# Optimization experiments

Measured on AMD Instinct MI355X. Metric: run time of the kernel, lower is better.

Reference implementation:

```python
import jax, jax.numpy as jnp
import numpy as np

N_JOINTS = 50
N_BONES = 50
# getSkeletalModelStructure() stand-in: 50 bones over 50 joints (i -> (i+1) % 50)
SRC = jnp.arange(N_BONES)
DST = (jnp.arange(N_BONES) + 1) % N_JOINTS
EPS = 1e-8


def _length_direct(x):
    # x: [B, T, 150] -> lengths [B, T, 50], directions [B, T, 150]
    B, T, _ = x.shape
    joints = x.reshape(B, T, N_JOINTS, 3)
    diff = joints[:, :, SRC, :] - joints[:, :, DST, :]      # [B, T, 50, 3]
    length = jnp.sqrt(jnp.sum(diff * diff, axis=-1))        # [B, T, 50]
    direct = diff / (length[..., None] + EPS)               # [B, T, 50, 3]
    return length, direct.reshape(B, T, N_BONES * 3)


def setup_inputs() -> dict:
    key = jax.random.key(0)
    k1, k2 = jax.random.split(key)
    preds = jax.random.normal(k1, (128, 1024, 150), dtype=jnp.float32)
    targets = jax.random.normal(k2, (128, 1024, 150), dtype=jnp.float32)
    return {"preds": preds, "targets": targets}


def reference(preds, targets):
    target_pad = 0.0
    loss_mask = (targets != target_pad).astype(jnp.float32)
    preds_masked = preds * loss_mask
    targets_masked = targets * loss_mask
    _, pd = _length_direct(preds_masked)
    _, td = _length_direct(targets_masked)
    pd = pd * loss_mask[:, :, :150]
    td = td * loss_mask[:, :, :150]
    # criterion = L1 (mean), criterion_bone = MSE (mean); loss_scale = 1.0
    loss = jnp.mean(jnp.abs(preds_masked - targets_masked)) + 0.1 * jnp.mean((pd - td) ** 2)
    return loss
```

## Files before the change

kernel.cpp:

```cpp
#include <hip/hip_runtime.h>


#define ROW_F   150
#define ROWS_PB 32
#define SPAN_F  (ROWS_PB * ROW_F)
#define SPAN_F4 (SPAN_F / 4)
#define N_CHUNK 19

typedef const __attribute__((address_space(1))) float  gfloat;
typedef __attribute__((address_space(3))) float        lfloat;

__global__ __launch_bounds__(256, 4) void loss_kernel(
    const float* __restrict__ preds,
    const float* __restrict__ targets,
    float* __restrict__ out,
    float inv_count)
{
    const float EPS = 1e-8f;
    __shared__ float sp[SPAN_F];
    __shared__ float st[SPAN_F];

    const int tid  = threadIdx.x;
    const int lane = tid & 63;
    const int wid  = tid >> 6;
    const size_t base = (size_t)blockIdx.x * SPAN_F;

    const float* gp = preds + base;
    const float* gt = targets + base;

    for (int c = wid; c < N_CHUNK; c += 4) {
        const int f4 = c * 64;
        if (f4 + lane < SPAN_F4) {
            __builtin_amdgcn_global_load_lds(
                (gfloat*)(gp + 4 * (f4 + lane)), (lfloat*)(sp + 4 * f4), 16, 0, 0);
            __builtin_amdgcn_global_load_lds(
                (gfloat*)(gt + 4 * (f4 + lane)), (lfloat*)(st + 4 * f4), 16, 0, 0);
        }
    }
    __syncthreads();

    const int seg = tid >> 5;
    const int row = tid & 31;
    const int j0 = (seg < 2) ? seg * 7 : 14 + (seg - 2) * 6;
    const int j1 = (seg < 2) ? j0 + 7  : j0 + 6;

    const float* rpb = sp + row * ROW_F;
    const float* rtb = st + row * ROW_F;

    float l1 = 0.0f, mse = 0.0f;

    auto load_joint = [&](int j, float* pm, float* tm, float* m) {
#pragma unroll
        for (int c = 0; c < 3; ++c) {
            float t = rtb[3 * j + c];
            float p = rpb[3 * j + c];
            float mk = (t != 0.0f) ? 1.0f : 0.0f;
            m[c] = mk;
            pm[c] = p * mk;
            tm[c] = t;
        }
    };

    auto do_bone = [&](const float* pmS, const float* tmS, const float* mS,
                       const float* pmD, const float* tmD) {
        float dp[3], dt[3];
        float lp = 0.0f, lt = 0.0f;
#pragma unroll
        for (int c = 0; c < 3; ++c) {
            dp[c] = pmS[c] - pmD[c];
            dt[c] = tmS[c] - tmD[c];
            lp += dp[c] * dp[c];
            lt += dt[c] * dt[c];
        }
        float ip = 1.0f / (sqrtf(lp) + EPS);
        float it = 1.0f / (sqrtf(lt) + EPS);
#pragma unroll
        for (int c = 0; c < 3; ++c) {
            float d = (dp[c] * ip - dt[c] * it) * mS[c];
            mse += d * d;
        }
    };

    float pmP[3], tmP[3], mP[3];
    load_joint(j0, pmP, tmP, mP);
#pragma unroll
    for (int c = 0; c < 3; ++c) l1 += fabsf(pmP[c] - tmP[c]);

    for (int b = j0; b < j1; ++b) {
        int jn = b + 1;
        if (jn == 50) jn = 0;
        float pmN[3], tmN[3], mN[3];
        load_joint(jn, pmN, tmN, mN);
        if (jn < j1 && jn != 0) {
#pragma unroll
            for (int c = 0; c < 3; ++c) l1 += fabsf(pmN[c] - tmN[c]);
        }
        do_bone(pmP, tmP, mP, pmN, tmN);
#pragma unroll
        for (int c = 0; c < 3; ++c) { pmP[c] = pmN[c]; tmP[c] = tmN[c]; mP[c] = mN[c]; }
    }

    float part = (l1 + 0.1f * mse) * inv_count;
#pragma unroll
    for (int off = 32; off > 0; off >>= 1)
        part += __shfl_down(part, off, 64);

    __shared__ float wsum[4];
    if (lane == 0) wsum[wid] = part;
    __syncthreads();
    if (tid == 0) {
        float s = wsum[0] + wsum[1] + wsum[2] + wsum[3];
        atomicAdd(out, s);
    }
}

extern "C" void kernel_launch(void* const* d_in, const int* in_sizes, int n_in,
                              void* d_out, int out_size, void* d_ws, size_t ws_size,
                              hipStream_t stream)
{
    const float* preds   = (const float*)d_in[0];
    const float* targets = (const float*)d_in[1];
    float* out = (float*)d_out;

    hipMemsetAsync(out, 0, sizeof(float) * out_size, stream);

    int n_elems = in_sizes[0];
    int n_rows  = n_elems / ROW_F;
    float inv_count = 1.0f / (float)n_elems;

    int grid = n_rows / ROWS_PB;
    loss_kernel<<<grid, 256, 0, stream>>>(preds, targets, out, inv_count);
}
```

Measured before the change: 184.3 us.

## Make loss kernel persistent with double-buffered LDS prefetch of spans

```diff
diff --git a/kernel.cpp b/kernel.cpp
--- a/kernel.cpp
+++ b/kernel.cpp
@@ -10,94 +10,107 @@
 typedef const __attribute__((address_space(1))) float  gfloat;
 typedef __attribute__((address_space(3))) float        lfloat;
 
-__global__ __launch_bounds__(256, 4) void loss_kernel(
+__device__ __forceinline__ void load_joint(const float* __restrict__ rpb,
+                                           const float* __restrict__ rtb,
+                                           int j, float* pm, float* tm, float* m)
+{
+#pragma unroll
+    for (int c = 0; c < 3; ++c) {
+        float t = rtb[3 * j + c];
+        float p = rpb[3 * j + c];
+        float mk = (t != 0.0f) ? 1.0f : 0.0f;
+        m[c] = mk;
+        pm[c] = p * mk;
+        tm[c] = t;
+    }
+}
+
+__device__ __forceinline__ void do_bone(const float* pmS, const float* tmS, const float* mS,
+                                        const float* pmD, const float* tmD, float& mse)
+{
+    const float EPS = 1e-8f;
+    float dp[3], dt[3];
+    float lp = 0.0f, lt = 0.0f;
+#pragma unroll
+    for (int c = 0; c < 3; ++c) {
+        dp[c] = pmS[c] - pmD[c];
+        dt[c] = tmS[c] - tmD[c];
+        lp += dp[c] * dp[c];
+        lt += dt[c] * dt[c];
+    }
+    float ip = 1.0f / (sqrtf(lp) + EPS);
+    float it = 1.0f / (sqrtf(lt) + EPS);
+#pragma unroll
+    for (int c = 0; c < 3; ++c) {
+        float d = (dp[c] * ip - dt[c] * it) * mS[c];
+        mse += d * d;
+    }
+}
+
+__global__ __launch_bounds__(256, 2) void loss_kernel(
     const float* __restrict__ preds,
     const float* __restrict__ targets,
     float* __restrict__ out,
-    float inv_count)
+    int iters, float inv_count)
 {
-    const float EPS = 1e-8f;
-    __shared__ float sp[SPAN_F];
-    __shared__ float st[SPAN_F];
+    __shared__ float smem[2][2][SPAN_F];
+    __shared__ float wsum[4];
 
     const int tid  = threadIdx.x;
     const int lane = tid & 63;
     const int wid  = tid >> 6;
-    const size_t base = (size_t)blockIdx.x * SPAN_F;
 
-    const float* gp = preds + base;
-    const float* gt = targets + base;
-
-    for (int c = wid; c < N_CHUNK; c += 4) {
-        const int f4 = c * 64;
-        if (f4 + lane < SPAN_F4) {
-            __builtin_amdgcn_global_load_lds(
-                (gfloat*)(gp + 4 * (f4 + lane)), (lfloat*)(sp + 4 * f4), 16, 0, 0);
-            __builtin_amdgcn_global_load_lds(
-                (gfloat*)(gt + 4 * (f4 + lane)), (lfloat*)(st + 4 * f4), 16, 0, 0);
+    auto stage = [&](int span, int buf) {
+        const float* gp = preds   + (size_t)span * SPAN_F;
+        const float* gt = targets + (size_t)span * SPAN_F;
+        float* bsp = smem[buf][0];
+        float* bst = smem[buf][1];
+        for (int c = wid; c < N_CHUNK; c += 4) {
+            const int f4 = c * 64;
+            if (f4 + lane < SPAN_F4) {
+                __builtin_amdgcn_global_load_lds(
+                    (gfloat*)(gp + 4 * (f4 + lane)), (lfloat*)(bsp + 4 * f4), 16, 0, 0);
+                __builtin_amdgcn_global_load_lds(
+                    (gfloat*)(gt + 4 * (f4 + lane)), (lfloat*)(bst + 4 * f4), 16, 0, 0);
+            }
         }
-    }
-    __syncthreads();
+    };
 
     const int seg = tid >> 5;
     const int row = tid & 31;
     const int j0 = (seg < 2) ? seg * 7 : 14 + (seg - 2) * 6;
     const int j1 = (seg < 2) ? j0 + 7  : j0 + 6;
 
-    const float* rpb = sp + row * ROW_F;
-    const float* rtb = st + row * ROW_F;
-
     float l1 = 0.0f, mse = 0.0f;
 
-    auto load_joint = [&](int j, float* pm, float* tm, float* m) {
+    stage(blockIdx.x, 0);
+
+    for (int it = 0; it < iters; ++it) {
+        __syncthreads();
+        if (it + 1 < iters)
+            stage(blockIdx.x + (it + 1) * gridDim.x, (it + 1) & 1);
+
+        const float* rpb = smem[it & 1][0] + row * ROW_F;
+        const float* rtb = smem[it & 1][1] + row * ROW_F;
+
+        float pmP[3], tmP[3], mP[3];
+        load_joint(rpb, rtb, j0, pmP, tmP, mP);
 #pragma unroll
-        for (int c = 0; c < 3; ++c) {
-            float t = rtb[3 * j + c];
-            float p = rpb[3 * j + c];
-            float mk = (t != 0.0f) ? 1.0f : 0.0f;
-            m[c] = mk;
-            pm[c] = p * mk;
-            tm[c] = t;
+        for (int c = 0; c < 3; ++c) l1 += fabsf(pmP[c] - tmP[c]);
+
+        for (int b = j0; b < j1; ++b) {
+            int jn = b + 1;
+            if (jn == 50) jn = 0;
+            float pmN[3], tmN[3], mN[3];
+            load_joint(rpb, rtb, jn, pmN, tmN, mN);
+            if (jn < j1 && jn != 0) {
+#pragma unroll
+                for (int c = 0; c < 3; ++c) l1 += fabsf(pmN[c] - tmN[c]);
+            }
+            do_bone(pmP, tmP, mP, pmN, tmN, mse);
+#pragma unroll
+            for (int c = 0; c < 3; ++c) { pmP[c] = pmN[c]; tmP[c] = tmN[c]; mP[c] = mN[c]; }
         }
-    };
-
-    auto do_bone = [&](const float* pmS, const float* tmS, const float* mS,
-                       const float* pmD, const float* tmD) {
-        float dp[3], dt[3];
-        float lp = 0.0f, lt = 0.0f;
-#pragma unroll
-        for (int c = 0; c < 3; ++c) {
-            dp[c] = pmS[c] - pmD[c];
-            dt[c] = tmS[c] - tmD[c];
-            lp += dp[c] * dp[c];
-            lt += dt[c] * dt[c];
-        }
-        float ip = 1.0f / (sqrtf(lp) + EPS);
-        float it = 1.0f / (sqrtf(lt) + EPS);
-#pragma unroll
-        for (int c = 0; c < 3; ++c) {
-            float d = (dp[c] * ip - dt[c] * it) * mS[c];
-            mse += d * d;
-        }
-    };
-
-    float pmP[3], tmP[3], mP[3];
-    load_joint(j0, pmP, tmP, mP);
-#pragma unroll
-    for (int c = 0; c < 3; ++c) l1 += fabsf(pmP[c] - tmP[c]);
-
-    for (int b = j0; b < j1; ++b) {
-        int jn = b + 1;
-        if (jn == 50) jn = 0;
-        float pmN[3], tmN[3], mN[3];
-        load_joint(jn, pmN, tmN, mN);
-        if (jn < j1 && jn != 0) {
-#pragma unroll
-            for (int c = 0; c < 3; ++c) l1 += fabsf(pmN[c] - tmN[c]);
-        }
-        do_bone(pmP, tmP, mP, pmN, tmN);
-#pragma unroll
-        for (int c = 0; c < 3; ++c) { pmP[c] = pmN[c]; tmP[c] = tmN[c]; mP[c] = mN[c]; }
     }
 
     float part = (l1 + 0.1f * mse) * inv_count;
@@ -105,7 +118,6 @@
     for (int off = 32; off > 0; off >>= 1)
         part += __shfl_down(part, off, 64);
 
-    __shared__ float wsum[4];
     if (lane == 0) wsum[wid] = part;
     __syncthreads();
     if (tid == 0) {
@@ -126,8 +138,10 @@
 
     int n_elems = in_sizes[0];
     int n_rows  = n_elems / ROW_F;
+    int spans   = n_rows / ROWS_PB;
     float inv_count = 1.0f / (float)n_elems;
 
-    int grid = n_rows / ROWS_PB;
-    loss_kernel<<<grid, 256, 0, stream>>>(preds, targets, out, inv_count);
+    int grid  = 512;
+    int iters = spans / grid;
+    loss_kernel<<<grid, 256, 0, stream>>>(preds, targets, out, iters, inv_count);
 }
```

Result: faster. 176.3 us (-4.3%).

## Make kernel persistent with register-prefetched spans and fast rcp/sqrt

Applied to the files above, without the earlier changes.

```diff
diff --git a/kernel.cpp b/kernel.cpp
--- a/kernel.cpp
+++ b/kernel.cpp
@@ -1,103 +1,114 @@
 #include <hip/hip_runtime.h>
 
 
-#define ROW_F   150
-#define ROWS_PB 32
-#define SPAN_F  (ROWS_PB * ROW_F)
-#define SPAN_F4 (SPAN_F / 4)
-#define N_CHUNK 19
-
-typedef const __attribute__((address_space(1))) float  gfloat;
-typedef __attribute__((address_space(3))) float        lfloat;
+#define ROW_F    150
+#define ROWS_PB  32
+#define SPAN_F   (ROWS_PB * ROW_F)
+#define SPAN_F4  (SPAN_F / 4)
+#define GRID     1024
 
 __global__ __launch_bounds__(256, 4) void loss_kernel(
     const float* __restrict__ preds,
     const float* __restrict__ targets,
     float* __restrict__ out,
-    float inv_count)
+    int iters, float inv_count)
 {
     const float EPS = 1e-8f;
     __shared__ float sp[SPAN_F];
     __shared__ float st[SPAN_F];
+    __shared__ float wsum[4];
 
     const int tid  = threadIdx.x;
     const int lane = tid & 63;
     const int wid  = tid >> 6;
-    const size_t base = (size_t)blockIdx.x * SPAN_F;
 
-    const float* gp = preds + base;
-    const float* gt = targets + base;
+    const float4* gp4 = reinterpret_cast<const float4*>(preds);
+    const float4* gt4 = reinterpret_cast<const float4*>(targets);
+    float4* sp4 = reinterpret_cast<float4*>(sp);
+    float4* st4 = reinterpret_cast<float4*>(st);
 
-    for (int c = wid; c < N_CHUNK; c += 4) {
-        const int f4 = c * 64;
-        if (f4 + lane < SPAN_F4) {
-            __builtin_amdgcn_global_load_lds(
-                (gfloat*)(gp + 4 * (f4 + lane)), (lfloat*)(sp + 4 * f4), 16, 0, 0);
-            __builtin_amdgcn_global_load_lds(
-                (gfloat*)(gt + 4 * (f4 + lane)), (lfloat*)(st + 4 * f4), 16, 0, 0);
-        }
-    }
-    __syncthreads();
+    const int g0 = tid, g1 = tid + 256, g2 = tid + 512, g3 = tid + 768, g4 = tid + 1024;
+    const bool w4 = (g4 < SPAN_F4);
+    const int g4c = w4 ? g4 : (SPAN_F4 - 1);
 
     const int seg = tid >> 5;
     const int row = tid & 31;
     const int j0 = (seg < 2) ? seg * 7 : 14 + (seg - 2) * 6;
     const int j1 = (seg < 2) ? j0 + 7  : j0 + 6;
 
-    const float* rpb = sp + row * ROW_F;
-    const float* rtb = st + row * ROW_F;
-
     float l1 = 0.0f, mse = 0.0f;
 
-    auto load_joint = [&](int j, float* pm, float* tm, float* m) {
+    size_t sb = (size_t)blockIdx.x * SPAN_F4;
+    float4 rp0 = gp4[sb + g0], rp1 = gp4[sb + g1], rp2 = gp4[sb + g2],
+           rp3 = gp4[sb + g3], rp4 = gp4[sb + g4c];
+    float4 rt0 = gt4[sb + g0], rt1 = gt4[sb + g1], rt2 = gt4[sb + g2],
+           rt3 = gt4[sb + g3], rt4 = gt4[sb + g4c];
+
+    for (int it = 0; it < iters; ++it) {
+        if (it) __syncthreads();
+
+        sp4[g0] = rp0; st4[g0] = rt0;
+        sp4[g1] = rp1; st4[g1] = rt1;
+        sp4[g2] = rp2; st4[g2] = rt2;
+        sp4[g3] = rp3; st4[g3] = rt3;
+        if (w4) { sp4[g4] = rp4; st4[g4] = rt4; }
+        __syncthreads();
+
+        if (it + 1 < iters) {
+            size_t nb = (size_t)(blockIdx.x + (size_t)(it + 1) * GRID) * SPAN_F4;
+            rp0 = gp4[nb + g0]; rp1 = gp4[nb + g1]; rp2 = gp4[nb + g2];
+            rp3 = gp4[nb + g3]; rp4 = gp4[nb + g4c];
+            rt0 = gt4[nb + g0]; rt1 = gt4[nb + g1]; rt2 = gt4[nb + g2];
+            rt3 = gt4[nb + g3]; rt4 = gt4[nb + g4c];
+        }
+
+        const float* rpb = sp + row * ROW_F;
+        const float* rtb = st + row * ROW_F;
+
+        float pmP[3], tmP[3];
 #pragma unroll
         for (int c = 0; c < 3; ++c) {
-            float t = rtb[3 * j + c];
-            float p = rpb[3 * j + c];
-            float mk = (t != 0.0f) ? 1.0f : 0.0f;
-            m[c] = mk;
-            pm[c] = p * mk;
-            tm[c] = t;
+            float t = rtb[3 * j0 + c];
+            float p = rpb[3 * j0 + c];
+            pmP[c] = (t != 0.0f) ? p : 0.0f;
+            tmP[c] = t;
+            l1 += fabsf(pmP[c] - tmP[c]);
         }
-    };
 
-    auto do_bone = [&](const float* pmS, const float* tmS, const float* mS,
-                       const float* pmD, const float* tmD) {
-        float dp[3], dt[3];
-        float lp = 0.0f, lt = 0.0f;
+        for (int b = j0; b < j1; ++b) {
+            int jn = b + 1;
+            if (jn == 50) jn = 0;
+            float pmN[3], tmN[3];
 #pragma unroll
-        for (int c = 0; c < 3; ++c) {
-            dp[c] = pmS[c] - pmD[c];
-            dt[c] = tmS[c] - tmD[c];
-            lp += dp[c] * dp[c];
-            lt += dt[c] * dt[c];
+            for (int c = 0; c < 3; ++c) {
+                float t = rtb[3 * jn + c];
+                float p = rpb[3 * jn + c];
+                pmN[c] = (t != 0.0f) ? p : 0.0f;
+                tmN[c] = t;
+            }
+            if (jn < j1 && jn != 0) {
+#pragma unroll
+                for (int c = 0; c < 3; ++c) l1 += fabsf(pmN[c] - tmN[c]);
+            }
+            float dp[3], dt[3], lp = 0.0f, lt = 0.0f;
+#pragma unroll
+            for (int c = 0; c < 3; ++c) {
+                dp[c] = pmP[c] - pmN[c];
+                dt[c] = tmP[c] - tmN[c];
+                lp += dp[c] * dp[c];
+                lt += dt[c] * dt[c];
+            }
+            float ip = __builtin_amdgcn_rcpf(__builtin_amdgcn_sqrtf(lp) + EPS);
+            float iq = __builtin_amdgcn_rcpf(__builtin_amdgcn_sqrtf(lt) + EPS);
+#pragma unroll
+            for (int c = 0; c < 3; ++c) {
+                float d = dp[c] * ip - dt[c] * iq;
+                d = (tmP[c] != 0.0f) ? d : 0.0f;
+                mse += d * d;
+            }
+#pragma unroll
+            for (int c = 0; c < 3; ++c) { pmP[c] = pmN[c]; tmP[c] = tmN[c]; }
         }
-        float ip = 1.0f / (sqrtf(lp) + EPS);
-        float it = 1.0f / (sqrtf(lt) + EPS);
-#pragma unroll
-        for (int c = 0; c < 3; ++c) {
-            float d = (dp[c] * ip - dt[c] * it) * mS[c];
-            mse += d * d;
-        }
-    };
-
-    float pmP[3], tmP[3], mP[3];
-    load_joint(j0, pmP, tmP, mP);
-#pragma unroll
-    for (int c = 0; c < 3; ++c) l1 += fabsf(pmP[c] - tmP[c]);
-
-    for (int b = j0; b < j1; ++b) {
-        int jn = b + 1;
-        if (jn == 50) jn = 0;
-        float pmN[3], tmN[3], mN[3];
-        load_joint(jn, pmN, tmN, mN);
-        if (jn < j1 && jn != 0) {
-#pragma unroll
-            for (int c = 0; c < 3; ++c) l1 += fabsf(pmN[c] - tmN[c]);
-        }
-        do_bone(pmP, tmP, mP, pmN, tmN);
-#pragma unroll
-        for (int c = 0; c < 3; ++c) { pmP[c] = pmN[c]; tmP[c] = tmN[c]; mP[c] = mN[c]; }
     }
 
     float part = (l1 + 0.1f * mse) * inv_count;
@@ -105,7 +116,6 @@
     for (int off = 32; off > 0; off >>= 1)
         part += __shfl_down(part, off, 64);
 
-    __shared__ float wsum[4];
     if (lane == 0) wsum[wid] = part;
     __syncthreads();
     if (tid == 0) {
@@ -126,8 +136,9 @@
 
     int n_elems = in_sizes[0];
     int n_rows  = n_elems / ROW_F;
+    int spans   = n_rows / ROWS_PB;
     float inv_count = 1.0f / (float)n_elems;
 
-    int grid = n_rows / ROWS_PB;
-    loss_kernel<<<grid, 256, 0, stream>>>(preds, targets, out, inv_count);
+    int iters = spans / GRID;
+    loss_kernel<<<GRID, 256, 0, stream>>>(preds, targets, out, iters, inv_count);
 }
```

Measured after the change: 175.6 us. -4.7%, faster.
